# Performance work log

Measured on AMD Instinct MI355X. Metric: run time of the kernel, lower is better.

## Reference

```python
import jax, jax.numpy as jnp
import numpy as np

TOP_K = 2  # cfg.MODEL.MOE.TOP_K


def setup_inputs() -> dict:
    key = jax.random.key(0)
    ks = jax.random.split(key, 5)
    bs, L, d_in, d_out, E = 32, 1024, 768, 256, 8
    return {
        "x": jax.random.normal(ks[0], (bs, L, d_in), dtype=jnp.float32),
        "gate_W": jax.random.normal(ks[1], (d_in, E), dtype=jnp.float32) * (1.0 / np.sqrt(d_in)),
        "gate_b": jax.random.normal(ks[2], (E,), dtype=jnp.float32) * 0.01,
        "expert_W": jax.random.normal(ks[3], (E, d_in, d_out), dtype=jnp.float32) * (1.0 / np.sqrt(d_in)),
        "expert_b": jax.random.normal(ks[4], (E, d_out), dtype=jnp.float32) * 0.01,
    }


def reference(x, gate_W, gate_b, expert_W, expert_b):
    # Gate: (bs, L, E) softmax over experts, then top-k routing weights.
    gate_logits = jnp.einsum("bli,ie->ble", x, gate_W) + gate_b
    gate_weights = jax.nn.softmax(gate_logits, axis=-1)
    topk_vals, topk_idx = jax.lax.top_k(gate_weights, TOP_K)  # (bs, L, K)

    # Dense all-expert projection (E is small), then gather the selected ones.
    # all_out: (bs, L, E, d_out)
    all_out = jnp.einsum("bli,eio->bleo", x, expert_W) + expert_b

    # Select top-k expert outputs per token: (bs, L, K, d_out)
    sel = jnp.take_along_axis(all_out, topk_idx[..., None], axis=2)

    # Weighted combine over the K routed experts -> (bs, L, d_out)
    output = jnp.sum(sel * topk_vals[..., None], axis=2)
    return output
```

## Files before the change

kernel.cpp:

```cpp
#include <hip/hip_runtime.h>
#include <hip/hip_bf16.h>
#include <stdint.h>

#define T_TOKENS 32768
#define D_IN     768
#define D_OUT    256
#define N_EXP    8
#define S_TOT    (T_TOKENS*2)
#define S_PAD    66560
#define KSPLIT   6
#define NKB      24

typedef __attribute__((ext_vector_type(8))) short bf16x8;
typedef __attribute__((ext_vector_type(4))) float f32x4;

__device__ __forceinline__ unsigned short f2bf(float f) {
    unsigned u = __float_as_uint(f);
    return (unsigned short)((u + 0x7FFFu + ((u >> 16) & 1u)) >> 16);
}
__device__ __forceinline__ unsigned pack_bf2(float a, float b) {
    return (unsigned)f2bf(a) | ((unsigned)f2bf(b) << 16);
}

__device__ __forceinline__ void async16(void* lds, const void* g) {
    __builtin_amdgcn_global_load_lds(
        (const __attribute__((address_space(1))) unsigned int*)g,
        (__attribute__((address_space(3))) unsigned int*)lds, 16, 0, 0);
}

__global__ __launch_bounds__(256) void convw_kernel(
        const float* __restrict__ W, unsigned short* __restrict__ WTb,
        int* __restrict__ zero16) {
    if (blockIdx.x == 0 && threadIdx.x < 16) zero16[threadIdx.x] = 0;
    int eb_ = blockIdx.x;
    int n = threadIdx.x;
    const float* src = W + ((size_t)(eb_ / NKB) * D_IN + (eb_ % NKB) * 32) * 256 + n;
    unsigned pk[16];
    #pragma unroll
    for (int j = 0; j < 16; j++)
        pk[j] = pack_bf2(src[(2*j) * 256], src[(2*j+1) * 256]);
    unsigned* dst = (unsigned*)(WTb + ((size_t)eb_ * 256 + n) * 32);
    #pragma unroll
    for (int j = 0; j < 16; j++) dst[j] = pk[j];
}

__global__ __launch_bounds__(64) void gate_partial_kernel(
        const float* __restrict__ x, const float* __restrict__ gW,
        unsigned short* __restrict__ xbf, float* __restrict__ partial) {
    __shared__ float tile[64 * 65];
    int tid = threadIdx.x;
    int t0  = blockIdx.x * 64;
    int kq  = blockIdx.y;
    int c16 = tid & 15, rb = tid >> 4;
    float acc[8] = {0,0,0,0,0,0,0,0};
    #pragma unroll 1
    for (int j = 0; j < 2; j++) {
        int kc = kq * 128 + j * 64;
        #pragma unroll
        for (int i = 0; i < 16; i++) {
            int row = i * 4 + rb;
            size_t g = (size_t)(t0 + row) * D_IN + kc + c16 * 4;
            float4 v = *(const float4*)(x + g);
            uint2 p; p.x = pack_bf2(v.x, v.y); p.y = pack_bf2(v.z, v.w);
            *(uint2*)(xbf + g) = p;
            float* d = &tile[row * 65 + c16 * 4];
            d[0] = v.x; d[1] = v.y; d[2] = v.z; d[3] = v.w;
        }
        __syncthreads();
        const float* gr = gW + (size_t)kc * 8;
        #pragma unroll 8
        for (int kk = 0; kk < 64; kk++) {
            float xv = tile[tid * 65 + kk];
            #pragma unroll
            for (int e = 0; e < 8; e++) acc[e] += xv * gr[kk * 8 + e];
        }
        __syncthreads();
    }
    float* dst = partial + ((size_t)kq * T_TOKENS + t0 + tid) * 8;
    float4 o0 = {acc[0], acc[1], acc[2], acc[3]};
    float4 o1 = {acc[4], acc[5], acc[6], acc[7]};
    *(float4*)dst = o0; *(float4*)(dst + 4) = o1;
}

__global__ __launch_bounds__(256) void gate_final_kernel(
        const float* __restrict__ partial, const float* __restrict__ gb,
        float* __restrict__ topk_w, int* __restrict__ topk_e, int* __restrict__ counts) {
    __shared__ int h[8];
    int tid = threadIdx.x;
    if (tid < 8) h[tid] = 0;
    __syncthreads();
    int t = blockIdx.x * 256 + tid;
    float acc[8] = {0,0,0,0,0,0,0,0};
    #pragma unroll
    for (int q = 0; q < KSPLIT; q++) {
        const float* p = partial + ((size_t)q * T_TOKENS + t) * 8;
        float4 a = *(const float4*)p;
        float4 b = *(const float4*)(p + 4);
        acc[0] += a.x; acc[1] += a.y; acc[2] += a.z; acc[3] += a.w;
        acc[4] += b.x; acc[5] += b.y; acc[6] += b.z; acc[7] += b.w;
    }
    float mx = -1e30f;
    #pragma unroll
    for (int e = 0; e < 8; e++) { acc[e] += gb[e]; mx = fmaxf(mx, acc[e]); }
    float w[8], s = 0.f;
    #pragma unroll
    for (int e = 0; e < 8; e++) { w[e] = expf(acc[e] - mx); s += w[e]; }
    float inv = 1.0f / s;
    int e0 = 0; float b0 = -1.f;
    #pragma unroll
    for (int e = 0; e < 8; e++) if (w[e] > b0) { b0 = w[e]; e0 = e; }
    int e1 = 0; float b1 = -1.f;
    #pragma unroll
    for (int e = 0; e < 8; e++) if (e != e0 && w[e] > b1) { b1 = w[e]; e1 = e; }
    topk_w[t*2]   = b0 * inv;
    topk_w[t*2+1] = b1 * inv;
    topk_e[t*2]   = e0;
    topk_e[t*2+1] = e1;
    atomicAdd(&h[e0], 1); atomicAdd(&h[e1], 1);
    __syncthreads();
    if (tid < 8) atomicAdd(&counts[tid], h[tid]);
}

__global__ void scatter_kernel(const int* __restrict__ topk_e, const float* __restrict__ topk_w,
                               const int* __restrict__ counts, int* __restrict__ cursors,
                               int* __restrict__ slot_token, float* __restrict__ slot_w,
                               int* __restrict__ inv_slot) {
    int offs[9]; offs[0] = 0;
    #pragma unroll
    for (int e = 0; e < 8; e++) offs[e+1] = offs[e] + ((counts[e] + 127) & ~127);
    __shared__ int hcnt[8], hbase[8];
    if (threadIdx.x < 8) hcnt[threadIdx.x] = 0;
    __syncthreads();
    int idx[4], ee[4], lr[4];
    int base = blockIdx.x * 256 * 4 + threadIdx.x;
    #pragma unroll
    for (int j = 0; j < 4; j++) {
        idx[j] = base + j * 256;
        ee[j]  = topk_e[idx[j]];
        lr[j]  = atomicAdd(&hcnt[ee[j]], 1);
    }
    __syncthreads();
    if (threadIdx.x < 8) hbase[threadIdx.x] = atomicAdd(&cursors[threadIdx.x], hcnt[threadIdx.x]);
    __syncthreads();
    #pragma unroll
    for (int j = 0; j < 4; j++) {
        int slot = offs[ee[j]] + hbase[ee[j]] + lr[j];
        slot_token[slot] = idx[j] >> 1;
        slot_w[slot]     = topk_w[idx[j]];
        inv_slot[idx[j]] = slot;
    }
}

template<bool ROUTED>
__global__ __launch_bounds__(256, 2) void moe_gemm_kernel(
        const unsigned short* __restrict__ xbf, const unsigned short* __restrict__ WTb,
        const float* __restrict__ eb, const int* __restrict__ counts,
        const int* __restrict__ slot_token, const float* __restrict__ slot_w,
        float* __restrict__ dst) {
    __shared__ unsigned short A_lds[3][128 * 32];
    __shared__ unsigned short B_lds[3][256 * 32];

    int offs[9]; offs[0] = 0;
    #pragma unroll
    for (int e = 0; e < 8; e++) offs[e+1] = offs[e] + ((counts[e] + 127) & ~127);
    int row0 = blockIdx.x * 128;
    if (row0 >= offs[8]) return;
    int expert = 0;
    #pragma unroll
    for (int e = 0; e < 8; e++) if (row0 >= offs[e]) expert = e;

    int tid  = threadIdx.x;
    int wave = tid >> 6, lane = tid & 63;
    int lrow = lane & 15, lquad = lane >> 4;

    const unsigned short* asrc[2];
    #pragma unroll
    for (int i = 0; i < 2; i++) {
        int c = i * 256 + tid;
        int r = c >> 2, p = c & 3;
        int lc = (p - (r >> 1)) & 3;
        int tok = slot_token[row0 + r];
        tok = (tok < 0 || tok >= T_TOKENS) ? 0 : tok;
        asrc[i] = xbf + (size_t)tok * D_IN + lc * 8;
    }
    const unsigned short* bexp = WTb + (size_t)expert * NKB * 8192;
    int boff[4];
    #pragma unroll
    for (int i = 0; i < 4; i++) {
        int c = i * 256 + tid;
        int r = c >> 2, p = c & 3;
        int lc = (p - (r >> 1)) & 3;
        boff[i] = r * 32 + lc * 8;
    }

    int a_off[8], b_off[4];
    #pragma unroll
    for (int m = 0; m < 8; m++) {
        int r = m * 16 + lrow;
        a_off[m] = r * 32 + ((lquad + (r >> 1)) & 3) * 8;
    }
    #pragma unroll
    for (int q = 0; q < 4; q++) {
        int r = wave * 64 + q * 16 + lrow;
        b_off[q] = r * 32 + ((lquad + (r >> 1)) & 3) * 8;
    }

    f32x4 acc[8][4];
    #pragma unroll
    for (int m = 0; m < 8; m++)
        #pragma unroll
        for (int q = 0; q < 4; q++) acc[m][q] = (f32x4){0,0,0,0};

    auto stage = [&](int kb, int st) {
        #pragma unroll
        for (int i = 0; i < 2; i++)
            async16(&A_lds[st][(i * 256 + tid) * 8], asrc[i] + kb * 32);
        const unsigned short* tb = bexp + (size_t)kb * 8192;
        #pragma unroll
        for (int i = 0; i < 4; i++)
            async16(&B_lds[st][(i * 256 + tid) * 8], tb + boff[i]);
    };

    stage(0, 0);
    stage(1, 1);
    for (int s = 0; s < NKB; s++) {
        if (s == NKB - 1) asm volatile("s_waitcnt vmcnt(0)" ::: "memory");
        else              asm volatile("s_waitcnt vmcnt(6)" ::: "memory");
        asm volatile("s_barrier" ::: "memory");
        if (s + 2 < NKB) stage(s + 2, (s + 2) % 3);
        int p = s % 3;
        bf16x8 a[8];
        #pragma unroll
        for (int m = 0; m < 8; m++) a[m] = *(const bf16x8*)&A_lds[p][a_off[m]];
        #pragma unroll
        for (int q = 0; q < 4; q++) {
            bf16x8 b = *(const bf16x8*)&B_lds[p][b_off[q]];
            #pragma unroll
            for (int m = 0; m < 8; m++)
                acc[m][q] = __builtin_amdgcn_mfma_f32_16x16x32_bf16(a[m], b, acc[m][q], 0, 0, 0);
        }
    }

    float bias_q[4];
    #pragma unroll
    for (int q = 0; q < 4; q++) bias_q[q] = eb[expert * D_OUT + wave * 64 + q * 16 + lrow];
    #pragma unroll
    for (int m = 0; m < 8; m++) {
        #pragma unroll
        for (int r = 0; r < 4; r++) {
            int slot = row0 + m * 16 + lquad * 4 + r;
            if constexpr (ROUTED) {
                float* drow = dst + (size_t)slot * D_OUT + wave * 64;
                #pragma unroll
                for (int q = 0; q < 4; q++)
                    drow[q * 16 + lrow] = acc[m][q][r] + bias_q[q];
            } else {
                int tk = slot_token[slot];
                float wgt = slot_w[slot];
                #pragma unroll
                for (int q = 0; q < 4; q++)
                    atomicAdd(dst + (size_t)tk * D_OUT + wave * 64 + q * 16 + lrow,
                              wgt * (acc[m][q][r] + bias_q[q]));
            }
        }
    }
}

__global__ void combine_kernel(const float* __restrict__ routed, const int* __restrict__ inv_slot,
                               const float* __restrict__ topk_w, float* __restrict__ out) {
    int flat = blockIdx.x * 256 + threadIdx.x;
    int t = flat >> 6, c = (flat & 63) * 4;
    int   s0 = inv_slot[t*2], s1 = inv_slot[t*2+1];
    float w0 = topk_w[t*2],   w1 = topk_w[t*2+1];
    float4 r0 = *(const float4*)(routed + (size_t)s0 * D_OUT + c);
    float4 r1 = *(const float4*)(routed + (size_t)s1 * D_OUT + c);
    float4 o;
    o.x = w0*r0.x + w1*r1.x; o.y = w0*r0.y + w1*r1.y;
    o.z = w0*r0.z + w1*r1.z; o.w = w0*r0.w + w1*r1.w;
    *(float4*)(out + (size_t)t * D_OUT + c) = o;
}

extern "C" void kernel_launch(void* const* d_in, const int* in_sizes, int n_in,
                              void* d_out, int out_size, void* d_ws, size_t ws_size,
                              hipStream_t stream) {
    const float* x  = (const float*)d_in[0];
    const float* gW = (const float*)d_in[1];
    const float* gb = (const float*)d_in[2];
    const float* eW = (const float*)d_in[3];
    const float* eb = (const float*)d_in[4];
    float* out = (float*)d_out;
    char* ws = (char*)d_ws;

    float* topk_w      = (float*)(ws + 0);
    int*   topk_e      = (int*)  (ws + 262144);
    int*   counts      = (int*)  (ws + 524288);
    int*   cursors     = (int*)  (ws + 524320);
    int*   slot_token  = (int*)  (ws + 524416);
    float* slot_w      = (float*)(ws + 790656);
    int*   inv_slot    = (int*)  (ws + 1056896);
    float* partial     = (float*)(ws + 1319040);
    unsigned short* WTb= (unsigned short*)(ws + 7610496);
    unsigned short* xbf= (unsigned short*)(ws + 10756224);
    float* routed      = (float*)(ws + 61087872);
    const size_t NEED_ROUTED = 61087872 + (size_t)S_PAD * D_OUT * 4;
    bool use_routed = (ws_size >= NEED_ROUTED);

    convw_kernel       <<<N_EXP * NKB, 256, 0, stream>>>(eW, WTb, counts);
    gate_partial_kernel<<<dim3(T_TOKENS / 64, KSPLIT), 64, 0, stream>>>(x, gW, xbf, partial);
    gate_final_kernel  <<<T_TOKENS / 256, 256, 0, stream>>>(partial, gb, topk_w, topk_e, counts);
    scatter_kernel     <<<S_TOT / (256 * 4), 256, 0, stream>>>(topk_e, topk_w, counts, cursors,
                                                               slot_token, slot_w, inv_slot);
    if (use_routed) {
        moe_gemm_kernel<true><<<S_PAD / 128, 256, 0, stream>>>(xbf, WTb, eb, counts,
                                                               slot_token, slot_w, routed);
        combine_kernel<<<T_TOKENS * D_OUT / 4 / 256, 256, 0, stream>>>(routed, inv_slot,
                                                                       topk_w, out);
    } else {
        hipMemsetAsync(slot_token, 0, 532480, stream);
        hipMemsetAsync(out, 0, (size_t)out_size * sizeof(float), stream);
        moe_gemm_kernel<false><<<S_PAD / 128, 256, 0, stream>>>(xbf, WTb, eb, counts,
                                                                slot_token, slot_w, out);
    }
}
```

Before: 269.2 us.

## Use 512-thread 2x4 wave tiling in MoE GEMM with block remap and setprio

Doubles the MoE GEMM block to 512 threads and arranges the waves as a 2x4 grid, so each wave computes a 64x64 sub-tile instead of 128x64. This halves the accumulators and A-fragment registers per wave, allowing more waves per CU, and each thread now issues fewer async loads per stage. Block indices are remapped so that consecutive hardware blocks are spread across the expert row ranges, and s_setprio is raised around the MFMA section. The cost is more waves contending for the barrier and smaller per-wave MFMA reuse. The remapped schedule also changes L2 locality for the expert weights.

Result: faster. 257.4 us (-4.4%).

```diff
diff --git a/kernel.cpp b/kernel.cpp
--- a/kernel.cpp
+++ b/kernel.cpp
@@ -152,7 +152,7 @@
 }
 
 template<bool ROUTED>
-__global__ __launch_bounds__(256, 2) void moe_gemm_kernel(
+__global__ __launch_bounds__(512, 4) void moe_gemm_kernel(
         const unsigned short* __restrict__ xbf, const unsigned short* __restrict__ WTb,
         const float* __restrict__ eb, const int* __restrict__ counts,
         const int* __restrict__ slot_token, const float* __restrict__ slot_w,
@@ -160,10 +160,12 @@
     __shared__ unsigned short A_lds[3][128 * 32];
     __shared__ unsigned short B_lds[3][256 * 32];
 
+    int lbid = (blockIdx.x & 7) * ((int)gridDim.x >> 3) + (blockIdx.x >> 3);
+
     int offs[9]; offs[0] = 0;
     #pragma unroll
     for (int e = 0; e < 8; e++) offs[e+1] = offs[e] + ((counts[e] + 127) & ~127);
-    int row0 = blockIdx.x * 128;
+    int row0 = lbid * 128;
     if (row0 >= offs[8]) return;
     int expert = 0;
     #pragma unroll
@@ -172,85 +174,82 @@
     int tid  = threadIdx.x;
     int wave = tid >> 6, lane = tid & 63;
     int lrow = lane & 15, lquad = lane >> 4;
-
-    const unsigned short* asrc[2];
+    int wm = wave >> 2, wn = wave & 3;
+
+    int ar = tid >> 2, ap = tid & 3;
+    int alc = (ap - (ar >> 1)) & 3;
+    int tok = slot_token[row0 + ar];
+    tok = (tok < 0 || tok >= T_TOKENS) ? 0 : tok;
+    const unsigned short* asrc = xbf + (size_t)tok * D_IN + alc * 8;
+
+    const unsigned short* bexp = WTb + (size_t)expert * NKB * 8192;
+    int boff[2];
     #pragma unroll
     for (int i = 0; i < 2; i++) {
-        int c = i * 256 + tid;
-        int r = c >> 2, p = c & 3;
-        int lc = (p - (r >> 1)) & 3;
-        int tok = slot_token[row0 + r];
-        tok = (tok < 0 || tok >= T_TOKENS) ? 0 : tok;
-        asrc[i] = xbf + (size_t)tok * D_IN + lc * 8;
-    }
-    const unsigned short* bexp = WTb + (size_t)expert * NKB * 8192;
-    int boff[4];
-    #pragma unroll
-    for (int i = 0; i < 4; i++) {
-        int c = i * 256 + tid;
+        int c = i * 512 + tid;
         int r = c >> 2, p = c & 3;
         int lc = (p - (r >> 1)) & 3;
         boff[i] = r * 32 + lc * 8;
     }
 
-    int a_off[8], b_off[4];
-    #pragma unroll
-    for (int m = 0; m < 8; m++) {
-        int r = m * 16 + lrow;
+    int a_off[4], b_off[4];
+    #pragma unroll
+    for (int m = 0; m < 4; m++) {
+        int r = wm * 64 + m * 16 + lrow;
         a_off[m] = r * 32 + ((lquad + (r >> 1)) & 3) * 8;
     }
     #pragma unroll
     for (int q = 0; q < 4; q++) {
-        int r = wave * 64 + q * 16 + lrow;
+        int r = wn * 64 + q * 16 + lrow;
         b_off[q] = r * 32 + ((lquad + (r >> 1)) & 3) * 8;
     }
 
-    f32x4 acc[8][4];
-    #pragma unroll
-    for (int m = 0; m < 8; m++)
+    f32x4 acc[4][4];
+    #pragma unroll
+    for (int m = 0; m < 4; m++)
         #pragma unroll
         for (int q = 0; q < 4; q++) acc[m][q] = (f32x4){0,0,0,0};
 
     auto stage = [&](int kb, int st) {
+        async16(&A_lds[st][tid * 8], asrc + kb * 32);
+        const unsigned short* tb = bexp + (size_t)kb * 8192;
         #pragma unroll
         for (int i = 0; i < 2; i++)
-            async16(&A_lds[st][(i * 256 + tid) * 8], asrc[i] + kb * 32);
-        const unsigned short* tb = bexp + (size_t)kb * 8192;
-        #pragma unroll
-        for (int i = 0; i < 4; i++)
-            async16(&B_lds[st][(i * 256 + tid) * 8], tb + boff[i]);
+            async16(&B_lds[st][(i * 512 + tid) * 8], tb + boff[i]);
     };
 
     stage(0, 0);
     stage(1, 1);
     for (int s = 0; s < NKB; s++) {
         if (s == NKB - 1) asm volatile("s_waitcnt vmcnt(0)" ::: "memory");
-        else              asm volatile("s_waitcnt vmcnt(6)" ::: "memory");
+        else              asm volatile("s_waitcnt vmcnt(3)" ::: "memory");
         asm volatile("s_barrier" ::: "memory");
         if (s + 2 < NKB) stage(s + 2, (s + 2) % 3);
         int p = s % 3;
-        bf16x8 a[8];
-        #pragma unroll
-        for (int m = 0; m < 8; m++) a[m] = *(const bf16x8*)&A_lds[p][a_off[m]];
-        #pragma unroll
-        for (int q = 0; q < 4; q++) {
-            bf16x8 b = *(const bf16x8*)&B_lds[p][b_off[q]];
+        bf16x8 a[4], b[4];
+        #pragma unroll
+        for (int m = 0; m < 4; m++) a[m] = *(const bf16x8*)&A_lds[p][a_off[m]];
+        #pragma unroll
+        for (int q = 0; q < 4; q++) b[q] = *(const bf16x8*)&B_lds[p][b_off[q]];
+        __builtin_amdgcn_s_setprio(1);
+        #pragma unroll
+        for (int q = 0; q < 4; q++)
             #pragma unroll
-            for (int m = 0; m < 8; m++)
-                acc[m][q] = __builtin_amdgcn_mfma_f32_16x16x32_bf16(a[m], b, acc[m][q], 0, 0, 0);
-        }
+            for (int m = 0; m < 4; m++)
+                acc[m][q] = __builtin_amdgcn_mfma_f32_16x16x32_bf16(a[m], b[q], acc[m][q], 0, 0, 0);
+        __builtin_amdgcn_s_setprio(0);
     }
 
     float bias_q[4];
     #pragma unroll
-    for (int q = 0; q < 4; q++) bias_q[q] = eb[expert * D_OUT + wave * 64 + q * 16 + lrow];
-    #pragma unroll
-    for (int m = 0; m < 8; m++) {
+    for (int q = 0; q < 4; q++) bias_q[q] = eb[expert * D_OUT + wn * 64 + q * 16 + lrow];
+    #pragma unroll
+    for (int m = 0; m < 4; m++) {
         #pragma unroll
         for (int r = 0; r < 4; r++) {
-            int slot = row0 + m * 16 + lquad * 4 + r;
+            int slot = row0 + wm * 64 + m * 16 + lquad * 4 + r;
             if constexpr (ROUTED) {
-                float* drow = dst + (size_t)slot * D_OUT + wave * 64;
+                float* drow = dst + (size_t)slot * D_OUT + wn * 64;
                 #pragma unroll
                 for (int q = 0; q < 4; q++)
                     drow[q * 16 + lrow] = acc[m][q][r] + bias_q[q];
@@ -259,7 +258,7 @@
                 float wgt = slot_w[slot];
                 #pragma unroll
                 for (int q = 0; q < 4; q++)
-                    atomicAdd(dst + (size_t)tk * D_OUT + wave * 64 + q * 16 + lrow,
+                    atomicAdd(dst + (size_t)tk * D_OUT + wn * 64 + q * 16 + lrow,
                               wgt * (acc[m][q][r] + bias_q[q]));
             }
         }
@@ -311,14 +310,14 @@
     scatter_kernel     <<<S_TOT / (256 * 4), 256, 0, stream>>>(topk_e, topk_w, counts, cursors,
                                                                slot_token, slot_w, inv_slot);
     if (use_routed) {
-        moe_gemm_kernel<true><<<S_PAD / 128, 256, 0, stream>>>(xbf, WTb, eb, counts,
+        moe_gemm_kernel<true><<<S_PAD / 128, 512, 0, stream>>>(xbf, WTb, eb, counts,
                                                                slot_token, slot_w, routed);
         combine_kernel<<<T_TOKENS * D_OUT / 4 / 256, 256, 0, stream>>>(routed, inv_slot,
                                                                        topk_w, out);
     } else {
         hipMemsetAsync(slot_token, 0, 532480, stream);
         hipMemsetAsync(out, 0, (size_t)out_size * sizeof(float), stream);
-        moe_gemm_kernel<false><<<S_PAD / 128, 256, 0, stream>>>(xbf, WTb, eb, counts,
+        moe_gemm_kernel<false><<<S_PAD / 128, 512, 0, stream>>>(xbf, WTb, eb, counts,
                                                                 slot_token, slot_w, out);
     }
 }
```
